# Kernel tuning notes

Hardware: AMD Instinct MI355X
Metric: run time of the kernel (lower is better)

## Reference

```python
import jax, jax.numpy as jnp
import numpy as np

B, S, E, H, I = 32, 257, 1024, 16, 4096
D = E // H  # head_dim = 64
EPS = 1e-5


def setup_inputs() -> dict:
    key = jax.random.key(0)
    ks = jax.random.split(key, 12)
    std = 0.02
    inp = {
        'hidden_states': jax.random.normal(ks[0], (B, S, E), jnp.float32),
        'attention_mask': jnp.zeros((B, 1, S, S), jnp.float32),
        'causal_attention_mask': jnp.zeros((B, 1, S, S), jnp.float32),
        'ln1_w': jnp.ones((E,), jnp.float32),
        'ln1_b': jnp.zeros((E,), jnp.float32),
        'q_w': jax.random.normal(ks[1], (E, E), jnp.float32) * std,
        'q_b': jnp.zeros((E,), jnp.float32),
        'k_w': jax.random.normal(ks[2], (E, E), jnp.float32) * std,
        'k_b': jnp.zeros((E,), jnp.float32),
        'v_w': jax.random.normal(ks[3], (E, E), jnp.float32) * std,
        'v_b': jnp.zeros((E,), jnp.float32),
        'o_w': jax.random.normal(ks[4], (E, E), jnp.float32) * std,
        'o_b': jnp.zeros((E,), jnp.float32),
        'ln2_w': jnp.ones((E,), jnp.float32),
        'ln2_b': jnp.zeros((E,), jnp.float32),
        'fc1_w': jax.random.normal(ks[5], (I, E), jnp.float32) * std,
        'fc1_b': jnp.zeros((I,), jnp.float32),
        'fc2_w': jax.random.normal(ks[6], (E, I), jnp.float32) * std,
        'fc2_b': jnp.zeros((E,), jnp.float32),
    }
    return inp


def _layernorm(x, w, b):
    mu = jnp.mean(x, axis=-1, keepdims=True)
    var = jnp.mean(jnp.square(x - mu), axis=-1, keepdims=True)
    return (x - mu) * jax.lax.rsqrt(var + EPS) * w + b


def _gelu_tanh(x):
    # 0.5*x*(1+tanh(sqrt(2/pi)*(x+0.044715*x^3)))
    c = np.sqrt(2.0 / np.pi).astype(np.float32)
    return 0.5 * x * (1.0 + jnp.tanh(c * (x + 0.044715 * x * x * x)))


def reference(hidden_states, attention_mask, causal_attention_mask,
              ln1_w, ln1_b, q_w, q_b, k_w, k_b, v_w, v_b, o_w, o_b,
              ln2_w, ln2_b, fc1_w, fc1_b, fc2_w, fc2_b):
    scale = D ** -0.5
    residual = hidden_states
    x = _layernorm(hidden_states, ln1_w, ln1_b)

    # projections (torch Linear: x @ W.T + b), q pre-scaled as in source
    q = (x @ q_w.T + q_b) * scale
    k = x @ k_w.T + k_b
    v = x @ v_w.T + v_b

    # [B, H, S, D]
    q = q.reshape(B, S, H, D).transpose(0, 2, 1, 3)
    k = k.reshape(B, S, H, D).transpose(0, 2, 1, 3)
    v = v.reshape(B, S, H, D).transpose(0, 2, 1, 3)

    scores = jnp.einsum('bhqd,bhkd->bhqk', q, k)  # [B,H,S,S]
    scores = scores + causal_attention_mask + attention_mask
    probs = jax.nn.softmax(scores, axis=-1)
    ctx = jnp.einsum('bhqk,bhkd->bhqd', probs, v)
    ctx = ctx.transpose(0, 2, 1, 3).reshape(B, S, E)
    attn_out = ctx @ o_w.T + o_b

    h = residual + attn_out
    residual = h
    x = _layernorm(h, ln2_w, ln2_b)
    x = _gelu_tanh(x @ fc1_w.T + fc1_b)
    x = x @ fc2_w.T + fc2_b
    return residual + x
```

## Files before the change

### kernel.cpp

```cpp
#include <hip/hip_runtime.h>

typedef unsigned short u16;
typedef unsigned int   u32;
typedef short s16x8 __attribute__((ext_vector_type(8)));
typedef float f32x4 __attribute__((ext_vector_type(4)));

#define MFMA16(A,B,C) __builtin_amdgcn_mfma_f32_16x16x32_bf16((A),(B),(C),0,0,0)
#define BAR() asm volatile("s_barrier" ::: "memory")

#define B_   32
#define S_   257
#define E_   1024
#define H_   16
#define D_   64
#define I_   4096
#define M_   (B_*S_)

__device__ __forceinline__ u16 f2bf(float f) {
    u32 u = __float_as_uint(f);
    u32 r = u + 0x7fffu + ((u >> 16) & 1u);
    return (u16)(r >> 16);
}
__device__ __forceinline__ float bf2f(u16 b) {
    return __uint_as_float(((u32)b) << 16);
}

__device__ __forceinline__ void gload16(const void* g, void* l) {
    __builtin_amdgcn_global_load_lds(
        (const __attribute__((address_space(1))) u32*)g,
        (__attribute__((address_space(3))) u32*)l, 16, 0, 0);
}

__global__ __launch_bounds__(256)
void convert_w_kernel(const float* __restrict__ qw, const float* __restrict__ kw,
                      const float* __restrict__ vw, const float* __restrict__ ow,
                      const float* __restrict__ f1, const float* __restrict__ f2,
                      u16* __restrict__ dst)
{
    const int total4 = (12 * 1048576) / 4;
    for (int i = blockIdx.x * 256 + threadIdx.x; i < total4; i += gridDim.x * 256) {
        int e = i * 4;
        int seg = e >> 20;
        const float* srcp; int off;
        if (seg < 4)      { srcp = (seg == 0 ? qw : seg == 1 ? kw : seg == 2 ? vw : ow); off = e & 1048575; }
        else if (seg < 8) { srcp = f1; off = e - 4 * 1048576; }
        else              { srcp = f2; off = e - 8 * 1048576; }
        float4 v = *(const float4*)(srcp + off);
        ushort4 o;
        o.x = f2bf(v.x); o.y = f2bf(v.y); o.z = f2bf(v.z); o.w = f2bf(v.w);
        *(ushort4*)(dst + e) = o;
    }
}

__global__ __launch_bounds__(256)
void mask_combine_kernel(const float* __restrict__ am, const float* __restrict__ cm,
                         u16* __restrict__ msum)
{
    const int total = B_ * S_ * 272;
    for (int i = blockIdx.x * 256 + threadIdx.x; i < total; i += gridDim.x * 256) {
        int skv = i % 272;
        int rem = i / 272;
        int sq  = rem % S_;
        int b   = rem / S_;
        float v;
        if (skv < S_) {
            size_t o = ((size_t)b * S_ + sq) * S_ + skv;
            v = am[o] + cm[o];
        } else v = -1e30f;
        msum[i] = f2bf(v);
    }
}

__global__ __launch_bounds__(256)
void ln_kernel(const float* __restrict__ src, const float* __restrict__ gam,
               const float* __restrict__ bet, u16* __restrict__ dst)
{
    int row = blockIdx.x;
    const float4* p = (const float4*)(src + (size_t)row * E_);
    float4 x = p[threadIdx.x];
    float s  = x.x + x.y + x.z + x.w;
    float s2 = x.x * x.x + x.y * x.y + x.z * x.z + x.w * x.w;
#pragma unroll
    for (int xm = 1; xm < 64; xm <<= 1) {
        s  += __shfl_xor(s,  xm, 64);
        s2 += __shfl_xor(s2, xm, 64);
    }
    __shared__ float red[8];
    int wv = threadIdx.x >> 6;
    if ((threadIdx.x & 63) == 0) { red[wv] = s; red[4 + wv] = s2; }
    __syncthreads();
    s  = red[0] + red[1] + red[2] + red[3];
    s2 = red[4] + red[5] + red[6] + red[7];
    float mu  = s * (1.0f / 1024.0f);
    float var = s2 * (1.0f / 1024.0f) - mu * mu;
    float rs  = rsqrtf(var + 1e-5f);
    float4 g  = ((const float4*)gam)[threadIdx.x];
    float4 be = ((const float4*)bet)[threadIdx.x];
    ushort4 o;
    o.x = f2bf((x.x - mu) * rs * g.x + be.x);
    o.y = f2bf((x.y - mu) * rs * g.y + be.y);
    o.z = f2bf((x.z - mu) * rs * g.z + be.z);
    o.w = f2bf((x.w - mu) * rs * g.w + be.w);
    ((ushort4*)dst)[(size_t)row * 256 + threadIdx.x] = o;
}

template<int MODE>
__global__ __launch_bounds__(512, 2)
void gemm8(const u16* __restrict__ A,
           const u16* __restrict__ Bq, const u16* __restrict__ Bk, const u16* __restrict__ Bv,
           const float* __restrict__ biasq, const float* __restrict__ biask, const float* __restrict__ biasvv,
           const float* __restrict__ res, float* __restrict__ outF,
           u16* __restrict__ outBq, u16* __restrict__ outBk, u16* __restrict__ outBv,
           int M, int N, int K)
{
    __shared__ u16 lds[8][4096];
    const int tid  = threadIdx.x;
    const int lane = tid & 63, w = tid >> 6;
    const int lr = lane & 15, lg = lane >> 4;
    const int wm = w >> 2, wn = w & 3;
    const int mt = blockIdx.y;

    const u16* Bm = Bq; const float* bias = biasq; u16* outB = outBq;
    float scl = 1.0f; int nt = blockIdx.x;
    if (MODE == 0) {
        int mat = nt >> 2; nt &= 3;
        if (mat == 1)      { Bm = Bk; bias = biask; outB = outBk; }
        else if (mat == 2) { Bm = Bv; bias = biasvv; outB = outBv; }
        if (mat == 0) scl = 0.125f;
    }
    const int m0 = mt * 256, n0 = nt * 256;
    const int NT = K >> 5;

    auto STAGE = [&](const u16* g, int grow0, int rowmax, int kt, int mat, int h) {
        char* dst = (char*)&lds[((kt & 1) << 2) + (mat << 1) + h][0] + w * 1024;
        int p = (w * 64 + lane) << 4;
        int l = p ^ (((p >> 7) & 3) << 4);
        int row = l >> 6, cc = (l >> 4) & 3;
        int gr = grow0 + row; if (gr > rowmax) gr = rowmax;
        gload16(g + (size_t)gr * K + (kt << 5) + cc * 8, dst);
    };
    const int swv = ((lr >> 1) & 3) << 4;
    auto LDA = [&](int kt, int mh, int mf) -> s16x8 {
        const char* base = (const char*)&lds[((kt & 1) << 2) + wm][0];
        return *(const s16x8*)(base + (mh * 64 + mf * 16 + lr) * 64 + ((lg * 16) ^ swv));
    };
    auto LDB = [&](int kt, int nh, int nf) -> s16x8 {
        const char* base = (const char*)&lds[((kt & 1) << 2) + 2 + (wn >> 1)][0];
        return *(const s16x8*)(base + ((wn & 1) * 64 + nh * 32 + nf * 16 + lr) * 64 + ((lg * 16) ^ swv));
    };

    f32x4 acc[8][4];
#pragma unroll
    for (int i = 0; i < 8; ++i)
#pragma unroll
        for (int j = 0; j < 4; ++j) { f32x4 z = {0.f, 0.f, 0.f, 0.f}; acc[i][j] = z; }

    STAGE(A,  m0,       M - 1, 0, 0, 0);
    STAGE(A,  m0 + 128, M - 1, 0, 0, 1);
    STAGE(Bm, n0,       N - 1, 0, 1, 0);
    STAGE(Bm, n0 + 128, N - 1, 0, 1, 1);
    if (NT > 1) {
        STAGE(A, m0, M - 1, 1, 0, 0);
        asm volatile("s_waitcnt vmcnt(1)" ::: "memory");
    } else {
        asm volatile("s_waitcnt vmcnt(0)" ::: "memory");
    }
    BAR();

    s16x8 aq[4], b0q[2], b1q[2];
    for (int kt = 0; kt < NT; ++kt) {
#pragma unroll
        for (int mf = 0; mf < 4; ++mf) aq[mf] = LDA(kt, 0, mf);
#pragma unroll
        for (int nf = 0; nf < 2; ++nf) b0q[nf] = LDB(kt, 0, nf);
        if (kt + 1 < NT) {
            STAGE(A,  m0 + 128, M - 1, kt + 1, 0, 1);
            STAGE(Bm, n0,       N - 1, kt + 1, 1, 0);
        }
        BAR();
        __builtin_amdgcn_s_setprio(1);
#pragma unroll
        for (int mf = 0; mf < 4; ++mf)
#pragma unroll
            for (int nf = 0; nf < 2; ++nf)
                acc[mf][nf] = MFMA16(aq[mf], b0q[nf], acc[mf][nf]);
        __builtin_amdgcn_s_setprio(0);
        BAR();
#pragma unroll
        for (int nf = 0; nf < 2; ++nf) b1q[nf] = LDB(kt, 1, nf);
        if (kt + 1 < NT) STAGE(Bm, n0 + 128, N - 1, kt + 1, 1, 1);
        BAR();
        __builtin_amdgcn_s_setprio(1);
#pragma unroll
        for (int mf = 0; mf < 4; ++mf)
#pragma unroll
            for (int nf = 0; nf < 2; ++nf)
                acc[mf][2 + nf] = MFMA16(aq[mf], b1q[nf], acc[mf][2 + nf]);
        __builtin_amdgcn_s_setprio(0);
        BAR();
#pragma unroll
        for (int mf = 0; mf < 4; ++mf) aq[mf] = LDA(kt, 1, mf);
        BAR();
        __builtin_amdgcn_s_setprio(1);
#pragma unroll
        for (int mf = 0; mf < 4; ++mf)
#pragma unroll
            for (int nf = 0; nf < 2; ++nf)
                acc[4 + mf][2 + nf] = MFMA16(aq[mf], b1q[nf], acc[4 + mf][2 + nf]);
        __builtin_amdgcn_s_setprio(0);
        BAR();
        if (kt + 2 < NT) STAGE(A, m0, M - 1, kt + 2, 0, 0);
        BAR();
        __builtin_amdgcn_s_setprio(1);
#pragma unroll
        for (int mf = 0; mf < 4; ++mf)
#pragma unroll
            for (int nf = 0; nf < 2; ++nf)
                acc[4 + mf][nf] = MFMA16(aq[mf], b0q[nf], acc[4 + mf][nf]);
        __builtin_amdgcn_s_setprio(0);
        if (kt + 1 < NT) {
            if (kt + 2 < NT) asm volatile("s_waitcnt vmcnt(1)" ::: "memory");
            else             asm volatile("s_waitcnt vmcnt(0)" ::: "memory");
        }
        BAR();
    }

    float biasv[4];
#pragma unroll
    for (int an = 0; an < 4; ++an) biasv[an] = bias[n0 + wn * 64 + an * 16 + lr];

#pragma unroll
    for (int am = 0; am < 8; ++am) {
#pragma unroll
        for (int r = 0; r < 4; ++r) {
            int row = m0 + wm * 128 + am * 16 + lg * 4 + r;
            if (row >= M) continue;
            if (MODE == 0) {
                int bb = row / S_;
                int ss = row - bb * S_;
#pragma unroll
                for (int an = 0; an < 4; ++an) {
                    int col = n0 + wn * 64 + an * 16 + lr;
                    int hh = col >> 6, dd = col & 63;
                    float v = (acc[am][an][r] + biasv[an]) * scl;
                    outB[(((size_t)bb * H_ + hh) * S_ + ss) * D_ + dd] = f2bf(v);
                }
            } else if (MODE == 1) {
                size_t base = (size_t)row * N;
#pragma unroll
                for (int an = 0; an < 4; ++an) {
                    int col = n0 + wn * 64 + an * 16 + lr;
                    outF[base + col] = acc[am][an][r] + biasv[an] + res[base + col];
                }
            } else {
                size_t base = (size_t)row * N;
#pragma unroll
                for (int an = 0; an < 4; ++an) {
                    int col = n0 + wn * 64 + an * 16 + lr;
                    float x = acc[am][an][r] + biasv[an];
                    float u = 0.7978845608028654f * (x + 0.044715f * x * x * x);
                    float t = tanhf(u);
                    outB[base + col] = f2bf(0.5f * x * (1.0f + t));
                }
            }
        }
    }
}

__global__ __launch_bounds__(256)
void attn_kernel(const u16* __restrict__ qg_, const u16* __restrict__ kg_,
                 const u16* __restrict__ vg_, const u16* __restrict__ msum,
                 u16* __restrict__ ctx)
{
    __shared__ u16 Ks[272 * 72];
    __shared__ u16 Vt[64 * 296];
    __shared__ u16 Ps[4][16 * 32];
    const int bh = blockIdx.x;
    const int b = bh >> 4, hh = bh & 15;
    const u16* kg = kg_ + (size_t)bh * (S_ * D_);
    const u16* vg = vg_ + (size_t)bh * (S_ * D_);
    const u16* qg = qg_ + (size_t)bh * (S_ * D_);
    const int tid = threadIdx.x, lane = tid & 63, wv = tid >> 6;

    for (int c = tid; c < (S_ * D_) / 8; c += 256) {
        int s = c >> 3, d8 = (c & 7) << 3;
        s16x8 val = *(const s16x8*)(kg + s * 64 + d8);
        *(s16x8*)&Ks[s * 72 + d8] = val;
    }
    for (int idx = tid; idx < 15 * 64; idx += 256) {
        int rr = 257 + (idx >> 6), cc = idx & 63;
        Ks[rr * 72 + cc] = 0;
    }
    for (int c = tid; c < (S_ * D_) / 8; c += 256) {
        int s = c >> 3, d8 = (c & 7) << 3;
        s16x8 val = *(const s16x8*)(vg + s * 64 + d8);
#pragma unroll
        for (int j = 0; j < 8; ++j) Vt[(d8 + j) * 296 + s] = (u16)val[j];
    }
    for (int idx = tid; idx < 64 * 39; idx += 256) {
        int dd = idx / 39, cc = 257 + idx % 39;
        Vt[dd * 296 + cc] = 0;
    }
    __syncthreads();

    const int lr = lane & 15, lg = lane >> 4;
    for (int qb = wv; qb < 17; qb += 4) {
        const int q0 = qb * 16;
        int qrow = q0 + lr; if (qrow > S_ - 1) qrow = S_ - 1;
        s16x8 aq0 = *(const s16x8*)(qg + qrow * 64 + lg * 8);
        s16x8 aq1 = *(const s16x8*)(qg + qrow * 64 + 32 + lg * 8);

        f32x4 sc[17];
#pragma unroll
        for (int t = 0; t < 17; ++t) { f32x4 z = {0.f, 0.f, 0.f, 0.f}; sc[t] = z; }
#pragma unroll
        for (int t = 0; t < 17; ++t) {
            s16x8 b0 = *(const s16x8*)&Ks[(t * 16 + lr) * 72 + lg * 8];
            s16x8 b1 = *(const s16x8*)&Ks[(t * 16 + lr) * 72 + 32 + lg * 8];
            sc[t] = MFMA16(aq0, b0, sc[t]);
            sc[t] = MFMA16(aq1, b1, sc[t]);
        }
        float mx[4] = {-3e38f, -3e38f, -3e38f, -3e38f};
#pragma unroll
        for (int r = 0; r < 4; ++r) {
            int sq = q0 + lg * 4 + r; if (sq > S_ - 1) sq = S_ - 1;
            const u16* mrow = msum + ((size_t)b * S_ + sq) * 272;
#pragma unroll
            for (int t = 0; t < 17; ++t) {
                sc[t][r] += bf2f(mrow[t * 16 + lr]);
                mx[r] = fmaxf(mx[r], sc[t][r]);
            }
        }
#pragma unroll
        for (int r = 0; r < 4; ++r) {
#pragma unroll
            for (int xm = 1; xm <= 8; xm <<= 1)
                mx[r] = fmaxf(mx[r], __shfl_xor(mx[r], xm, 64));
        }
        float sum[4] = {0.f, 0.f, 0.f, 0.f};
#pragma unroll
        for (int t = 0; t < 17; ++t)
#pragma unroll
            for (int r = 0; r < 4; ++r) {
                float e = __expf(sc[t][r] - mx[r]);
                sc[t][r] = e; sum[r] += e;
            }
#pragma unroll
        for (int r = 0; r < 4; ++r) {
#pragma unroll
            for (int xm = 1; xm <= 8; xm <<= 1)
                sum[r] += __shfl_xor(sum[r], xm, 64);
        }

        f32x4 ac[4];
#pragma unroll
        for (int nt = 0; nt < 4; ++nt) { f32x4 z = {0.f, 0.f, 0.f, 0.f}; ac[nt] = z; }
        u16* myP = &Ps[wv][0];
#pragma unroll
        for (int kc = 0; kc < 9; ++kc) {
#pragma unroll
            for (int tt = 0; tt < 2; ++tt) {
                const int t = kc * 2 + tt;
#pragma unroll
                for (int r = 0; r < 4; ++r) {
                    float pv = (t < 17) ? sc[(t < 17) ? t : 0][r] : 0.f;
                    myP[(lg * 4 + r) * 32 + tt * 16 + lr] = f2bf(pv);
                }
            }
            s16x8 pa = *(const s16x8*)&myP[lr * 32 + lg * 8];
#pragma unroll
            for (int nt = 0; nt < 4; ++nt) {
                s16x8 bv = *(const s16x8*)&Vt[(nt * 16 + lr) * 296 + kc * 32 + lg * 8];
                ac[nt] = MFMA16(pa, bv, ac[nt]);
            }
        }
#pragma unroll
        for (int r = 0; r < 4; ++r) {
            int sq = q0 + lg * 4 + r;
            if (sq < S_) {
                float rd = 1.0f / sum[r];
                size_t base = (((size_t)b * S_ + sq) * H_ + hh) * D_;
#pragma unroll
                for (int nt = 0; nt < 4; ++nt)
                    ctx[base + nt * 16 + lr] = f2bf(ac[nt][r] * rd);
            }
        }
    }
}

extern "C" void kernel_launch(void* const* d_in, const int* in_sizes, int n_in,
                              void* d_out, int out_size, void* d_ws, size_t ws_size,
                              hipStream_t stream)
{
    const float* hid   = (const float*)d_in[0];
    const float* am    = (const float*)d_in[1];
    const float* cm    = (const float*)d_in[2];
    const float* ln1w  = (const float*)d_in[3];
    const float* ln1b  = (const float*)d_in[4];
    const float* qw    = (const float*)d_in[5];
    const float* qbias = (const float*)d_in[6];
    const float* kw    = (const float*)d_in[7];
    const float* kbias = (const float*)d_in[8];
    const float* vw    = (const float*)d_in[9];
    const float* vbias = (const float*)d_in[10];
    const float* ow    = (const float*)d_in[11];
    const float* obias = (const float*)d_in[12];
    const float* ln2w  = (const float*)d_in[13];
    const float* ln2b  = (const float*)d_in[14];
    const float* f1w   = (const float*)d_in[15];
    const float* f1b   = (const float*)d_in[16];
    const float* f2w   = (const float*)d_in[17];
    const float* f2b   = (const float*)d_in[18];
    float* out = (float*)d_out;

    const size_t ME = (size_t)M_ * E_;
    u16* Wq   = (u16*)d_ws;
    u16* Wk   = Wq + 1048576;
    u16* Wv   = Wk + 1048576;
    u16* Wo   = Wv + 1048576;
    u16* Wf1  = Wo + 1048576;
    u16* Wf2  = Wf1 + 4 * 1048576;
    u16* xln  = Wf2 + 4 * 1048576;
    u16* qb_  = xln + ME;
    u16* kb_  = qb_ + ME;
    u16* vb_  = kb_ + ME;
    u16* ctx  = vb_ + ME;
    float* hbuf = (float*)(ctx + ME);
    u16* msum = (u16*)(hbuf + ME);
    u16* act  = qb_;
    u16* x2   = xln;

    convert_w_kernel<<<3072, 256, 0, stream>>>(qw, kw, vw, ow, f1w, f2w, Wq);
    mask_combine_kernel<<<8736, 256, 0, stream>>>(am, cm, msum);
    ln_kernel<<<M_, 256, 0, stream>>>(hid, ln1w, ln1b, xln);
    gemm8<0><<<dim3(12, 33), 512, 0, stream>>>(xln, Wq, Wk, Wv, qbias, kbias, vbias,
                                               nullptr, nullptr, qb_, kb_, vb_,
                                               M_, 1024, 1024);
    attn_kernel<<<512, 256, 0, stream>>>(qb_, kb_, vb_, msum, ctx);
    gemm8<1><<<dim3(4, 33), 512, 0, stream>>>(ctx, Wo, nullptr, nullptr, obias, nullptr, nullptr,
                                              hid, hbuf, nullptr, nullptr, nullptr,
                                              M_, 1024, 1024);
    ln_kernel<<<M_, 256, 0, stream>>>(hbuf, ln2w, ln2b, x2);
    gemm8<2><<<dim3(16, 33), 512, 0, stream>>>(x2, Wf1, nullptr, nullptr, f1b, nullptr, nullptr,
                                               nullptr, nullptr, act, nullptr, nullptr,
                                               M_, 4096, 1024);
    gemm8<1><<<dim3(4, 33), 512, 0, stream>>>(act, Wf2, nullptr, nullptr, f2b, nullptr, nullptr,
                                              hbuf, out, nullptr, nullptr, nullptr,
                                              M_, 1024, 4096);
}
```

Baseline: 464.4 us.

## Deepen GEMM K-tile to 64 and split-K the FC2 projection

Restructures the GEMM mainloop to stage 64-wide K tiles (double-buffered, 8-way XOR swizzle) with two MFMAs per fragment pair, halving the number of barrier-bounded iterations. It also adds a split-K mode for FC2 that writes two fp32 partial buffers, then a separate reduce kernel adds the partials, bias and residual. This is meant to cut per-iteration sync overhead and to fix the low occupancy of the 132-block FC2 grid. The cost is doubled LDS usage, two extra full-size fp32 writes and reads for the partials, and one extra kernel launch.

```diff
diff --git a/kernel.cpp b/kernel.cpp
--- a/kernel.cpp
+++ b/kernel.cpp
@@ -6,7 +6,10 @@
 typedef float f32x4 __attribute__((ext_vector_type(4)));
 
 #define MFMA16(A,B,C) __builtin_amdgcn_mfma_f32_16x16x32_bf16((A),(B),(C),0,0,0)
-#define BAR() asm volatile("s_barrier" ::: "memory")
+#define BAR()  asm volatile("s_barrier" ::: "memory")
+#define LGKM0  asm volatile("s_waitcnt lgkmcnt(0)" ::: "memory")
+#define VMC2   asm volatile("s_waitcnt vmcnt(2)" ::: "memory")
+#define VMC0   asm volatile("s_waitcnt vmcnt(0)" ::: "memory")
 
 #define B_   32
 #define S_   257
@@ -109,44 +112,55 @@
 void gemm8(const u16* __restrict__ A,
            const u16* __restrict__ Bq, const u16* __restrict__ Bk, const u16* __restrict__ Bv,
            const float* __restrict__ biasq, const float* __restrict__ biask, const float* __restrict__ biasvv,
-           const float* __restrict__ res, float* __restrict__ outF,
+           const float* __restrict__ res, float* __restrict__ outF, float* __restrict__ outF1,
            u16* __restrict__ outBq, u16* __restrict__ outBk, u16* __restrict__ outBv,
-           int M, int N, int K)
-{
-    __shared__ u16 lds[8][4096];
-    const int tid  = threadIdx.x;
-    const int lane = tid & 63, w = tid >> 6;
+           int M, int N, int Ks, int klen)
+{
+    __shared__ u16 lds[2][4][8192];
+    const int tid = threadIdx.x, lane = tid & 63, w = tid >> 6;
     const int lr = lane & 15, lg = lane >> 4;
     const int wm = w >> 2, wn = w & 3;
-    const int mt = blockIdx.y;
 
     const u16* Bm = Bq; const float* bias = biasq; u16* outB = outBq;
-    float scl = 1.0f; int nt = blockIdx.x;
+    float scl = 1.0f; int nt = blockIdx.x; int k0 = 0; float* outP = outF;
     if (MODE == 0) {
         int mat = nt >> 2; nt &= 3;
         if (mat == 1)      { Bm = Bk; bias = biask; outB = outBk; }
         else if (mat == 2) { Bm = Bv; bias = biasvv; outB = outBv; }
         if (mat == 0) scl = 0.125f;
-    }
-    const int m0 = mt * 256, n0 = nt * 256;
-    const int NT = K >> 5;
-
-    auto STAGE = [&](const u16* g, int grow0, int rowmax, int kt, int mat, int h) {
-        char* dst = (char*)&lds[((kt & 1) << 2) + (mat << 1) + h][0] + w * 1024;
-        int p = (w * 64 + lane) << 4;
-        int l = p ^ (((p >> 7) & 3) << 4);
-        int row = l >> 6, cc = (l >> 4) & 3;
-        int gr = grow0 + row; if (gr > rowmax) gr = rowmax;
-        gload16(g + (size_t)gr * K + (kt << 5) + cc * 8, dst);
+    } else if (MODE == 3) {
+        int kz = nt & 1; nt >>= 1;
+        k0 = kz * klen;
+        if (kz) outP = outF1;
+    }
+    const int m0 = blockIdx.y * 256, n0 = nt * 256;
+    const int NT = klen >> 6, NI = klen >> 7;
+    const int tb = k0 >> 6;
+
+    {
+    }
+    const int p    = w * 1024 + lane * 16;
+    const int lby  = p ^ (((p >> 7) & 7) << 4);
+    const int srow = lby >> 7;
+    const int scol = (lby & 127) >> 1;
+
+    auto STAGE = [&](int buf, int half, const u16* src, int grow0, int rowmax, int t) {
+#pragma unroll
+        for (int s = 0; s < 2; ++s) {
+            int gr = grow0 + s * 64 + srow; if (gr > rowmax) gr = rowmax;
+            gload16(src + (size_t)gr * Ks + ((tb + t) << 6) + scol,
+                    (char*)&lds[buf][half][0] + s * 8192 + w * 1024);
+        }
     };
-    const int swv = ((lr >> 1) & 3) << 4;
-    auto LDA = [&](int kt, int mh, int mf) -> s16x8 {
-        const char* base = (const char*)&lds[((kt & 1) << 2) + wm][0];
-        return *(const s16x8*)(base + (mh * 64 + mf * 16 + lr) * 64 + ((lg * 16) ^ swv));
+    auto LDA = [&](int buf, int mh, int mf, int kh) -> s16x8 {
+        const char* b = (const char*)&lds[buf][wm][0];
+        int inrow = mh * 64 + mf * 16 + lr;
+        return *(const s16x8*)(b + inrow * 128 + ((kh * 64 + lg * 16) ^ ((lr & 7) << 4)));
     };
-    auto LDB = [&](int kt, int nh, int nf) -> s16x8 {
-        const char* base = (const char*)&lds[((kt & 1) << 2) + 2 + (wn >> 1)][0];
-        return *(const s16x8*)(base + ((wn & 1) * 64 + nh * 32 + nf * 16 + lr) * 64 + ((lg * 16) ^ swv));
+    auto LDB = [&](int buf, int nh, int nf, int kh) -> s16x8 {
+        const char* b = (const char*)&lds[buf][2 + (wn >> 1)][0];
+        int inrow = (wn & 1) * 64 + nh * 32 + nf * 16 + lr;
+        return *(const s16x8*)(b + inrow * 128 + ((kh * 64 + lg * 16) ^ ((lr & 7) << 4)));
     };
 
     f32x4 acc[8][4];
@@ -155,92 +169,115 @@
 #pragma unroll
         for (int j = 0; j < 4; ++j) { f32x4 z = {0.f, 0.f, 0.f, 0.f}; acc[i][j] = z; }
 
-    STAGE(A,  m0,       M - 1, 0, 0, 0);
-    STAGE(A,  m0 + 128, M - 1, 0, 0, 1);
-    STAGE(Bm, n0,       N - 1, 0, 1, 0);
-    STAGE(Bm, n0 + 128, N - 1, 0, 1, 1);
-    if (NT > 1) {
-        STAGE(A, m0, M - 1, 1, 0, 0);
-        asm volatile("s_waitcnt vmcnt(1)" ::: "memory");
-    } else {
-        asm volatile("s_waitcnt vmcnt(0)" ::: "memory");
-    }
+    s16x8 a[4][2], b[2][2][2];
+    auto MFQ = [&](int mh, int nh) {
+        __builtin_amdgcn_s_setprio(1);
+#pragma unroll
+        for (int mf = 0; mf < 4; ++mf)
+#pragma unroll
+            for (int nf = 0; nf < 2; ++nf)
+#pragma unroll
+                for (int kh = 0; kh < 2; ++kh)
+                    acc[mh * 4 + mf][nh * 2 + nf] =
+                        MFMA16(a[mf][kh], b[nh][nf][kh], acc[mh * 4 + mf][nh * 2 + nf]);
+        __builtin_amdgcn_s_setprio(0);
+    };
+
+    STAGE(0, 0, A,  m0,       M - 1, 0);
+    STAGE(0, 1, A,  m0 + 128, M - 1, 0);
+    STAGE(0, 2, Bm, n0,       N - 1, 0);
+    STAGE(0, 3, Bm, n0 + 128, N - 1, 0);
+    STAGE(1, 0, A,  m0,       M - 1, 1);
+    VMC2;
     BAR();
 
-    s16x8 aq[4], b0q[2], b1q[2];
-    for (int kt = 0; kt < NT; ++kt) {
-#pragma unroll
-        for (int mf = 0; mf < 4; ++mf) aq[mf] = LDA(kt, 0, mf);
-#pragma unroll
-        for (int nf = 0; nf < 2; ++nf) b0q[nf] = LDB(kt, 0, nf);
-        if (kt + 1 < NT) {
-            STAGE(A,  m0 + 128, M - 1, kt + 1, 0, 1);
-            STAGE(Bm, n0,       N - 1, kt + 1, 1, 0);
-        }
-        BAR();
-        __builtin_amdgcn_s_setprio(1);
+    for (int i = 0; i < NI; ++i) {
+        const int t1 = 2 * i + 1, t2 = 2 * i + 2, t3 = 2 * i + 3;
+        const bool more = (i + 1 < NI);
 #pragma unroll
         for (int mf = 0; mf < 4; ++mf)
 #pragma unroll
-            for (int nf = 0; nf < 2; ++nf)
-                acc[mf][nf] = MFMA16(aq[mf], b0q[nf], acc[mf][nf]);
-        __builtin_amdgcn_s_setprio(0);
-        BAR();
-#pragma unroll
-        for (int nf = 0; nf < 2; ++nf) b1q[nf] = LDB(kt, 1, nf);
-        if (kt + 1 < NT) STAGE(Bm, n0 + 128, N - 1, kt + 1, 1, 1);
-        BAR();
-        __builtin_amdgcn_s_setprio(1);
+            for (int kh = 0; kh < 2; ++kh) a[mf][kh] = LDA(0, 0, mf, kh);
+#pragma unroll
+        for (int nf = 0; nf < 2; ++nf)
+#pragma unroll
+            for (int kh = 0; kh < 2; ++kh) b[0][nf][kh] = LDB(0, 0, nf, kh);
+        STAGE(1, 1, A, m0 + 128, M - 1, t1);
+        BAR(); LGKM0;
+        MFQ(0, 0);
+        BAR();
+#pragma unroll
+        for (int nf = 0; nf < 2; ++nf)
+#pragma unroll
+            for (int kh = 0; kh < 2; ++kh) b[1][nf][kh] = LDB(0, 1, nf, kh);
+        STAGE(1, 2, Bm, n0, N - 1, t1);
+        BAR(); LGKM0;
+        MFQ(0, 1);
+        BAR();
 #pragma unroll
         for (int mf = 0; mf < 4; ++mf)
 #pragma unroll
-            for (int nf = 0; nf < 2; ++nf)
-                acc[mf][2 + nf] = MFMA16(aq[mf], b1q[nf], acc[mf][2 + nf]);
-        __builtin_amdgcn_s_setprio(0);
-        BAR();
-#pragma unroll
-        for (int mf = 0; mf < 4; ++mf) aq[mf] = LDA(kt, 1, mf);
-        BAR();
-        __builtin_amdgcn_s_setprio(1);
+            for (int kh = 0; kh < 2; ++kh) a[mf][kh] = LDA(0, 1, mf, kh);
+        STAGE(1, 3, Bm, n0 + 128, N - 1, t1);
+        BAR(); LGKM0;
+        MFQ(1, 1);
+        BAR();
+        if (more) STAGE(0, 0, A, m0, M - 1, t2);
+        MFQ(1, 0);
+        if (more) { VMC2; } else { VMC0; }
+        BAR();
 #pragma unroll
         for (int mf = 0; mf < 4; ++mf)
 #pragma unroll
-            for (int nf = 0; nf < 2; ++nf)
-                acc[4 + mf][2 + nf] = MFMA16(aq[mf], b1q[nf], acc[4 + mf][2 + nf]);
-        __builtin_amdgcn_s_setprio(0);
-        BAR();
-        if (kt + 2 < NT) STAGE(A, m0, M - 1, kt + 2, 0, 0);
-        BAR();
-        __builtin_amdgcn_s_setprio(1);
+            for (int kh = 0; kh < 2; ++kh) a[mf][kh] = LDA(1, 0, mf, kh);
+#pragma unroll
+        for (int nf = 0; nf < 2; ++nf)
+#pragma unroll
+            for (int kh = 0; kh < 2; ++kh) b[0][nf][kh] = LDB(1, 0, nf, kh);
+        if (more) STAGE(0, 2, Bm, n0, N - 1, t2);
+        BAR(); LGKM0;
+        MFQ(0, 0);
+        BAR();
+#pragma unroll
+        for (int nf = 0; nf < 2; ++nf)
+#pragma unroll
+            for (int kh = 0; kh < 2; ++kh) b[1][nf][kh] = LDB(1, 1, nf, kh);
+        if (more) STAGE(0, 3, Bm, n0 + 128, N - 1, t2);
+        BAR(); LGKM0;
+        MFQ(0, 1);
+        BAR();
 #pragma unroll
         for (int mf = 0; mf < 4; ++mf)
 #pragma unroll
-            for (int nf = 0; nf < 2; ++nf)
-                acc[4 + mf][nf] = MFMA16(aq[mf], b0q[nf], acc[4 + mf][nf]);
-        __builtin_amdgcn_s_setprio(0);
-        if (kt + 1 < NT) {
-            if (kt + 2 < NT) asm volatile("s_waitcnt vmcnt(1)" ::: "memory");
-            else             asm volatile("s_waitcnt vmcnt(0)" ::: "memory");
-        }
+            for (int kh = 0; kh < 2; ++kh) a[mf][kh] = LDA(1, 1, mf, kh);
+        if (more) STAGE(0, 1, A, m0 + 128, M - 1, t2);
+        BAR(); LGKM0;
+        MFQ(1, 1);
+        BAR();
+        if (more) STAGE(1, 0, A, m0, M - 1, t3);
+        MFQ(1, 0);
+        if (more) VMC2;
         BAR();
     }
 
     float biasv[4];
-#pragma unroll
-    for (int an = 0; an < 4; ++an) biasv[an] = bias[n0 + wn * 64 + an * 16 + lr];
-
+    if (MODE != 3) {
+#pragma unroll
+        for (int an = 0; an < 4; ++an)
+            biasv[an] = bias[n0 + wn * 64 + (an >> 1) * 32 + (an & 1) * 16 + lr];
+    }
 #pragma unroll
     for (int am = 0; am < 8; ++am) {
 #pragma unroll
         for (int r = 0; r < 4; ++r) {
-            int row = m0 + wm * 128 + am * 16 + lg * 4 + r;
+            int row = m0 + wm * 128 + (am >> 2) * 64 + (am & 3) * 16 + lg * 4 + r;
             if (row >= M) continue;
             if (MODE == 0) {
                 int bb = row / S_;
                 int ss = row - bb * S_;
 #pragma unroll
                 for (int an = 0; an < 4; ++an) {
-                    int col = n0 + wn * 64 + an * 16 + lr;
+                    int col = n0 + wn * 64 + (an >> 1) * 32 + (an & 1) * 16 + lr;
                     int hh = col >> 6, dd = col & 63;
                     float v = (acc[am][an][r] + biasv[an]) * scl;
                     outB[(((size_t)bb * H_ + hh) * S_ + ss) * D_ + dd] = f2bf(v);
@@ -249,21 +286,48 @@
                 size_t base = (size_t)row * N;
 #pragma unroll
                 for (int an = 0; an < 4; ++an) {
-                    int col = n0 + wn * 64 + an * 16 + lr;
+                    int col = n0 + wn * 64 + (an >> 1) * 32 + (an & 1) * 16 + lr;
                     outF[base + col] = acc[am][an][r] + biasv[an] + res[base + col];
                 }
-            } else {
+            } else if (MODE == 2) {
                 size_t base = (size_t)row * N;
 #pragma unroll
                 for (int an = 0; an < 4; ++an) {
-                    int col = n0 + wn * 64 + an * 16 + lr;
+                    int col = n0 + wn * 64 + (an >> 1) * 32 + (an & 1) * 16 + lr;
                     float x = acc[am][an][r] + biasv[an];
                     float u = 0.7978845608028654f * (x + 0.044715f * x * x * x);
                     float t = tanhf(u);
                     outB[base + col] = f2bf(0.5f * x * (1.0f + t));
                 }
+            } else {
+                size_t base = (size_t)row * N;
+#pragma unroll
+                for (int an = 0; an < 4; ++an) {
+                    int col = n0 + wn * 64 + (an >> 1) * 32 + (an & 1) * 16 + lr;
+                    outP[base + col] = acc[am][an][r];
+                }
             }
         }
+    }
+}
+
+__global__ __launch_bounds__(256)
+void fc2_reduce(const float* __restrict__ P0, const float* __restrict__ P1,
+                const float* __restrict__ res, const float* __restrict__ bias,
+                float* __restrict__ out)
+{
+    const int n4 = (M_ * E_) / 4;
+    for (int i = blockIdx.x * 256 + threadIdx.x; i < n4; i += gridDim.x * 256) {
+        float4 x0 = ((const float4*)P0)[i];
+        float4 x1 = ((const float4*)P1)[i];
+        float4 rr = ((const float4*)res)[i];
+        float4 bb = ((const float4*)bias)[i & 255];
+        float4 o;
+        o.x = x0.x + x1.x + rr.x + bb.x;
+        o.y = x0.y + x1.y + rr.y + bb.y;
+        o.z = x0.z + x1.z + rr.z + bb.z;
+        o.w = x0.w + x1.w + rr.w + bb.w;
+        ((float4*)out)[i] = o;
     }
 }
 
@@ -429,22 +493,33 @@
     u16* msum = (u16*)(hbuf + ME);
     u16* act  = qb_;
     u16* x2   = xln;
+    float* P0 = (float*)(msum + (size_t)B_ * S_ * 272);
+    float* P1 = P0 + ME;
+    const size_t need = (size_t)((char*)(P1 + ME) - (char*)d_ws);
+    const bool split = ws_size >= need;
 
     convert_w_kernel<<<3072, 256, 0, stream>>>(qw, kw, vw, ow, f1w, f2w, Wq);
     mask_combine_kernel<<<8736, 256, 0, stream>>>(am, cm, msum);
     ln_kernel<<<M_, 256, 0, stream>>>(hid, ln1w, ln1b, xln);
     gemm8<0><<<dim3(12, 33), 512, 0, stream>>>(xln, Wq, Wk, Wv, qbias, kbias, vbias,
-                                               nullptr, nullptr, qb_, kb_, vb_,
-                                               M_, 1024, 1024);
+                                               nullptr, nullptr, nullptr, qb_, kb_, vb_,
+                                               M_, 1024, 1024, 1024);
     attn_kernel<<<512, 256, 0, stream>>>(qb_, kb_, vb_, msum, ctx);
     gemm8<1><<<dim3(4, 33), 512, 0, stream>>>(ctx, Wo, nullptr, nullptr, obias, nullptr, nullptr,
-                                              hid, hbuf, nullptr, nullptr, nullptr,
-                                              M_, 1024, 1024);
+                                              hid, hbuf, nullptr, nullptr, nullptr, nullptr,
+                                              M_, 1024, 1024, 1024);
     ln_kernel<<<M_, 256, 0, stream>>>(hbuf, ln2w, ln2b, x2);
     gemm8<2><<<dim3(16, 33), 512, 0, stream>>>(x2, Wf1, nullptr, nullptr, f1b, nullptr, nullptr,
-                                               nullptr, nullptr, act, nullptr, nullptr,
-                                               M_, 4096, 1024);
-    gemm8<1><<<dim3(4, 33), 512, 0, stream>>>(act, Wf2, nullptr, nullptr, f2b, nullptr, nullptr,
-                                              hbuf, out, nullptr, nullptr, nullptr,
-                                              M_, 1024, 4096);
-}
+                                               nullptr, nullptr, nullptr, act, nullptr, nullptr,
+                                               M_, 4096, 1024, 1024);
+    if (split) {
+        gemm8<3><<<dim3(8, 33), 512, 0, stream>>>(act, Wf2, nullptr, nullptr, nullptr, nullptr, nullptr,
+                                                  nullptr, P0, P1, nullptr, nullptr, nullptr,
+                                                  M_, 1024, 4096, 2048);
+        fc2_reduce<<<2048, 256, 0, stream>>>(P0, P1, hbuf, f2b, out);
+    } else {
+        gemm8<1><<<dim3(4, 33), 512, 0, stream>>>(act, Wf2, nullptr, nullptr, f2b, nullptr, nullptr,
+                                                  hbuf, out, nullptr, nullptr, nullptr, nullptr,
+                                                  M_, 1024, 4096, 4096);
+    }
+}
```

After: 451.2 us. 1.03x faster.
